# Kernel tuning notes

Hardware: AMD Instinct MI355X
Metric: run time of the kernel (lower is better)

The kernel has to match this reference:

```python
import jax, jax.numpy as jnp
import numpy as np

B, S, D, H, W = 2, 2048, 1024, 16, 256
HD = D // H

def setup_inputs() -> dict:
    key = jax.random.key(0)
    k1, k2, k3 = jax.random.split(key, 3)
    x = jax.random.normal(k1, (B, S, D), dtype=jnp.float32)
    w_qkv = jax.random.normal(k2, (D, 3 * D), dtype=jnp.float32) * (D ** -0.5)
    b_qkv = jnp.zeros((3 * D,), dtype=jnp.float32)
    w_out = jax.random.normal(k3, (D, D), dtype=jnp.float32) * (D ** -0.5)
    b_out = jnp.zeros((D,), dtype=jnp.float32)
    return {"x": x, "w_qkv": w_qkv, "b_qkv": b_qkv, "w_out": w_out, "b_out": b_out}

def reference(x, w_qkv, b_qkv, w_out, b_out):
    b, s, d = x.shape
    qkv = x @ w_qkv + b_qkv                       # [B,S,3D]
    qkv = qkv.reshape(b, s, 3, H, HD)
    q = jnp.transpose(qkv[:, :, 0], (0, 2, 1, 3))  # [B,H,S,HD]
    k = jnp.transpose(qkv[:, :, 1], (0, 2, 1, 3))
    v = jnp.transpose(qkv[:, :, 2], (0, 2, 1, 3))
    # NOTE: original scales by d_model**0.5, not head_dim**0.5
    scores = jnp.einsum('bhqd,bhkd->bhqk', q, k) / (d ** 0.5)
    idx = jnp.arange(s)
    band = jnp.abs(idx[:, None] - idx[None, :]) <= W  # |i-j| <= window_size
    scores = jnp.where(band[None, None], scores, -jnp.inf)
    attn = jax.nn.softmax(scores, axis=-1)
    out = jnp.einsum('bhqk,bhkd->bhqd', attn, v)
    out = jnp.transpose(out, (0, 2, 1, 3)).reshape(b, s, d)
    return out @ w_out + b_out
```

## Files before the change

### kernel.cpp

```cpp
#include <hip/hip_runtime.h>
#include <cstdint>
#include <cmath>

typedef unsigned short u16;
typedef __attribute__((ext_vector_type(8))) short bf16x8;
typedef __attribute__((ext_vector_type(4))) float f32x4;
typedef __attribute__((ext_vector_type(8))) unsigned short u16x8;

#define DEV static __device__ __forceinline__

DEV u16 f2bf(float f) {
  union { float f; uint32_t u; } v; v.f = f;
  uint32_t r = (v.u + 0x7fffu + ((v.u >> 16) & 1u)) >> 16;
  return (u16)r;
}

DEV float fexp2(float x) { return exp2f(x); }

DEV void async16(void* lds, const void* g) {
  __builtin_amdgcn_global_load_lds(
      (const __attribute__((address_space(1))) uint32_t*)g,
      (__attribute__((address_space(3))) uint32_t*)lds, 16, 0, 0);
}

__global__ void conv8(const float* __restrict__ in, u16* __restrict__ out, int n8) {
  int i = blockIdx.x * 256 + threadIdx.x;
  if (i >= n8) return;
  const float4* p = (const float4*)in + (size_t)i * 2;
  float4 a = p[0], b = p[1];
  u16x8 ov;
  ov[0] = f2bf(a.x); ov[1] = f2bf(a.y); ov[2] = f2bf(a.z); ov[3] = f2bf(a.w);
  ov[4] = f2bf(b.x); ov[5] = f2bf(b.y); ov[6] = f2bf(b.z); ov[7] = f2bf(b.w);
  *(u16x8*)(out + (size_t)i * 8) = ov;
}

__global__ void tconv(const float* __restrict__ in, u16* __restrict__ out, int R, int Cdim) {
  __shared__ float t[32][33];
  const int tx = threadIdx.x & 31, ty = threadIdx.x >> 5;
  const int r0 = blockIdx.y * 32, c0 = blockIdx.x * 32;
#pragma unroll
  for (int k = 0; k < 4; ++k) {
    int r = ty + k * 8;
    t[r][tx] = in[(size_t)(r0 + r) * Cdim + c0 + tx];
  }
  __syncthreads();
#pragma unroll
  for (int k = 0; k < 4; ++k) {
    int cc = ty + k * 8;
    out[(size_t)(c0 + cc) * R + r0 + tx] = f2bf(t[tx][cc]);
  }
}

template <int EPI>
__global__ __launch_bounds__(256, 2) void gemm_bt(
    const u16* __restrict__ A, const u16* __restrict__ BT,
    const float* __restrict__ bias, float* __restrict__ C,
    u16* __restrict__ qb, u16* __restrict__ kbuf, u16* __restrict__ vtb,
    int Mdim, int Ndim, int Kdim)
{
  __shared__ u16 Alds[128 * 64];
  __shared__ u16 Blds[128 * 64];
  const int tid = threadIdx.x;
  const int wid = tid >> 6, lane = tid & 63;
  const int g = lane >> 4, c = lane & 15;
  const int wr = wid >> 1, wc = wid & 1;
  const int gx = gridDim.x;
  const int nwg = gx * gridDim.y;
  const int lin = blockIdx.y * gx + blockIdx.x;
  const int work = (lin & 7) * (nwg >> 3) + (lin >> 3);
  const int row0 = (work / gx) * 128, col0 = (work % gx) * 128;

  f32x4 acc[4][4] = {};

  for (int kt = 0; kt < Kdim; kt += 64) {
    __syncthreads();
#pragma unroll
    for (int it = 0; it < 4; ++it) {
      int chunk = wid * 256 + it * 64 + lane;
      int r = chunk >> 3, j = chunk & 7;
      int js = j ^ (r & 7);
      async16((char*)Alds + (wid * 256 + it * 64) * 16,
              A + (size_t)(row0 + r) * Kdim + kt + js * 8);
      async16((char*)Blds + (wid * 256 + it * 64) * 16,
              BT + (size_t)(col0 + r) * Kdim + kt + js * 8);
    }
    __syncthreads();
#pragma unroll
    for (int kk = 0; kk < 2; ++kk) {
      bf16x8 av[4], bv[4];
#pragma unroll
      for (int mi = 0; mi < 4; ++mi) {
        int r = wr * 64 + mi * 16 + c;
        int js = (kk * 4 + g) ^ (r & 7);
        av[mi] = *(const bf16x8*)((const char*)Alds + r * 128 + js * 16);
      }
#pragma unroll
      for (int ni = 0; ni < 4; ++ni) {
        int r = wc * 64 + ni * 16 + c;
        int js = (kk * 4 + g) ^ (r & 7);
        bv[ni] = *(const bf16x8*)((const char*)Blds + r * 128 + js * 16);
      }
#pragma unroll
      for (int mi = 0; mi < 4; ++mi)
#pragma unroll
        for (int ni = 0; ni < 4; ++ni)
          acc[mi][ni] = __builtin_amdgcn_mfma_f32_16x16x32_bf16(
              av[mi], bv[ni], acc[mi][ni], 0, 0, 0);
    }
  }

#pragma unroll
  for (int mi = 0; mi < 4; ++mi) {
#pragma unroll
    for (int ni = 0; ni < 4; ++ni) {
      int colg = col0 + wc * 64 + ni * 16 + c;
      float bsv = bias[colg];
#pragma unroll
      for (int r = 0; r < 4; ++r) {
        int rowg = row0 + wr * 64 + mi * 16 + g * 4 + r;
        float val = acc[mi][ni][r] + bsv;
        if (EPI == 0) {
          C[(size_t)rowg * Ndim + colg] = val;
        } else {
          int t = colg >> 10, rem = colg & 1023;
          int h = rem >> 6, hd = rem & 63;
          int b = rowg >> 11, s = rowg & 2047;
          size_t bho = (size_t)(b * 16 + h);
          u16 bvv = f2bf(val);
          if (t == 0)      qb  [(bho * 2048 + s) * 64 + hd] = bvv;
          else if (t == 1) kbuf[(bho * 2048 + s) * 64 + hd] = bvv;
          else             vtb [(bho * 64 + hd) * 2048 + s] = bvv;
        }
      }
    }
  }
}

__global__ __launch_bounds__(512, 4) void attn_win(
    const u16* __restrict__ qb, const u16* __restrict__ kb,
    const u16* __restrict__ vtb, u16* __restrict__ hb)
{
  constexpr int S = 2048, W = 256;
  __shared__ u16 Klds[2][64 * 64];
  __shared__ u16 Vlds[2][64 * 64];
  __shared__ u16 Plds[8][16 * 64];

  const int tid = threadIdx.x, wid = tid >> 6, lane = tid & 63;
  const int g = lane >> 4, c = lane & 15;
  const int lin = blockIdx.x;
  const int work = (lin & 7) * 64 + (lin >> 3);
  const int qt = work & 15, bh = work >> 4;
  const int q0 = qt * 128;
  const int qr0 = q0 + wid * 16;
  const size_t bho = (size_t)bh * S * 64;

  bf16x8 aq[2];
  {
    const u16* qrow = qb + bho + (size_t)(qr0 + c) * 64;
    aq[0] = *(const bf16x8*)(qrow + g * 8);
    aq[1] = *(const bf16x8*)(qrow + 32 + g * 8);
  }
  f32x4 o[4] = {};
  float m[4] = {-1e30f, -1e30f, -1e30f, -1e30f};
  float lsum[4] = {0.f, 0.f, 0.f, 0.f};

  const int kstart = (q0 - W > 0) ? (q0 - W) : 0;
  const int kend = (q0 + 128 + W < S) ? (q0 + 128 + W) : S;
  constexpr float kS = 0.04508422002778011f;

  const int sr = tid >> 3, sj = tid & 7;
  const int sjs = sj ^ (sr & 7);
#define STAGE(buf, k0s)                                                         \
  {                                                                             \
    async16((char*)&Klds[buf][0] + tid * 16,                                    \
            kb + bho + (size_t)((k0s) + sr) * 64 + sjs * 8);                    \
    async16((char*)&Vlds[buf][0] + tid * 16,                                    \
            vtb + bho + (size_t)sr * S + (k0s) + sjs * 8);                      \
  }

  STAGE(0, kstart);
  asm volatile("s_waitcnt vmcnt(0)" ::: "memory");
  __syncthreads();

  int cur = 0;
  for (int k0 = kstart; k0 < kend; k0 += 64) {
    if (k0 + 64 < kend) STAGE(cur ^ 1, k0 + 64);

    const bool wave_active = !(k0 > qr0 + 15 + W) && !(k0 + 63 < qr0 - W);
    if (wave_active) {
      const u16* Kb = &Klds[cur][0];
      const u16* Vb = &Vlds[cur][0];

      f32x4 sacc[4] = {};
#pragma unroll
      for (int kb4 = 0; kb4 < 4; ++kb4) {
        int krow = kb4 * 16 + c;
#pragma unroll
        for (int kk = 0; kk < 2; ++kk) {
          int js = (kk * 4 + g) ^ (krow & 7);
          bf16x8 bk = *(const bf16x8*)((const char*)Kb + krow * 128 + js * 16);
          sacc[kb4] = __builtin_amdgcn_mfma_f32_16x16x32_bf16(aq[kk], bk, sacc[kb4], 0, 0, 0);
        }
      }

      const bool full = (k0 >= qr0 + 15 - W) && (k0 + 63 <= qr0 + W);
      float sl[4][4];
      if (full) {
#pragma unroll
        for (int kb4 = 0; kb4 < 4; ++kb4)
#pragma unroll
          for (int r = 0; r < 4; ++r) sl[kb4][r] = sacc[kb4][r] * kS;
      } else {
#pragma unroll
        for (int kb4 = 0; kb4 < 4; ++kb4) {
          int key = k0 + kb4 * 16 + c;
#pragma unroll
          for (int r = 0; r < 4; ++r) {
            int d = qr0 + g * 4 + r - key;
            bool valid = (d <= W) && (d >= -W);
            sl[kb4][r] = valid ? sacc[kb4][r] * kS : -1e30f;
          }
        }
      }

      float pmax[4];
#pragma unroll
      for (int r = 0; r < 4; ++r) {
        float mx = fmaxf(fmaxf(sl[0][r], sl[1][r]), fmaxf(sl[2][r], sl[3][r]));
        mx = fmaxf(mx, __shfl_xor(mx, 1));
        mx = fmaxf(mx, __shfl_xor(mx, 2));
        mx = fmaxf(mx, __shfl_xor(mx, 4));
        mx = fmaxf(mx, __shfl_xor(mx, 8));
        pmax[r] = mx;
      }
      float grow = fmaxf(fmaxf(pmax[0] - m[0], pmax[1] - m[1]),
                         fmaxf(pmax[2] - m[2], pmax[3] - m[3]));
      if (!__all(grow <= 8.0f)) {
#pragma unroll
        for (int r = 0; r < 4; ++r) {
          float mnew = fmaxf(m[r], pmax[r]);
          float fs = fexp2(m[r] - mnew);
          m[r] = mnew;
          lsum[r] *= fs;
          o[0][r] *= fs; o[1][r] *= fs; o[2][r] *= fs; o[3][r] *= fs;
        }
      }

      float rowsum[4] = {0.f, 0.f, 0.f, 0.f};
      u16* Pw = &Plds[wid][0];
#pragma unroll
      for (int kb4 = 0; kb4 < 4; ++kb4) {
#pragma unroll
        for (int r = 0; r < 4; ++r) {
          float p;
          if (full) {
            p = fexp2(sl[kb4][r] - m[r]);
          } else {
            p = (sl[kb4][r] > -1e29f) ? fexp2(sl[kb4][r] - m[r]) : 0.0f;
          }
          rowsum[r] += p;
          int row = g * 4 + r;
          int key = kb4 * 16 + c;
          int jsw = (key >> 3) ^ (row & 7);
          *((u16*)((char*)Pw + row * 128 + jsw * 16 + (key & 7) * 2)) = f2bf(p);
        }
      }
#pragma unroll
      for (int r = 0; r < 4; ++r) {
        float s2 = rowsum[r];
        s2 += __shfl_xor(s2, 1);
        s2 += __shfl_xor(s2, 2);
        s2 += __shfl_xor(s2, 4);
        s2 += __shfl_xor(s2, 8);
        lsum[r] += s2;
      }
      asm volatile("s_waitcnt lgkmcnt(0)" ::: "memory");
      __builtin_amdgcn_sched_barrier(0);
#pragma unroll
      for (int ks = 0; ks < 2; ++ks) {
        int js = (ks * 4 + g) ^ (c & 7);
        bf16x8 pa = *(const bf16x8*)((const char*)Pw + c * 128 + js * 16);
#pragma unroll
        for (int nb = 0; nb < 4; ++nb) {
          int hd = nb * 16 + c;
          int vjs = (ks * 4 + g) ^ (hd & 7);
          bf16x8 bv = *(const bf16x8*)((const char*)Vb + hd * 128 + vjs * 16);
          o[nb] = __builtin_amdgcn_mfma_f32_16x16x32_bf16(pa, bv, o[nb], 0, 0, 0);
        }
      }
    }

    asm volatile("s_waitcnt vmcnt(0)" ::: "memory");
    __syncthreads();
    cur ^= 1;
  }
#undef STAGE

  const int b = bh >> 4, h = bh & 15;
#pragma unroll
  for (int r = 0; r < 4; ++r) {
    float inv = 1.0f / lsum[r];
    int qr = qr0 + g * 4 + r;
#pragma unroll
    for (int nb = 0; nb < 4; ++nb) {
      int col = h * 64 + nb * 16 + c;
      hb[(size_t)(b * 2048 + qr) * 1024 + col] = f2bf(o[nb][r] * inv);
    }
  }
}

extern "C" void kernel_launch(void* const* d_in, const int* in_sizes, int n_in,
                              void* d_out, int out_size, void* d_ws, size_t ws_size,
                              hipStream_t stream) {
  const float* x     = (const float*)d_in[0];
  const float* w_qkv = (const float*)d_in[1];
  const float* b_qkv = (const float*)d_in[2];
  const float* w_out = (const float*)d_in[3];
  const float* b_out = (const float*)d_in[4];
  float* out = (float*)d_out;

  char* ws = (char*)d_ws;
  const size_t MB = 1024 * 1024;
  u16* xbf   = (u16*)(ws);
  u16* wqT   = (u16*)(ws + 8 * MB);
  u16* woT   = (u16*)(ws + 14 * MB);
  u16* qbuf  = (u16*)(ws + 16 * MB);
  u16* kbuf  = (u16*)(ws + 24 * MB);
  u16* vtbuf = (u16*)(ws + 32 * MB);
  u16* hbuf  = (u16*)(ws + 40 * MB);

  conv8<<<dim3(4096 * 1024 / 8 / 256), 256, 0, stream>>>(x, xbf, 4096 * 1024 / 8);
  tconv<<<dim3(3072 / 32, 1024 / 32), 256, 0, stream>>>(w_qkv, wqT, 1024, 3072);
  tconv<<<dim3(1024 / 32, 1024 / 32), 256, 0, stream>>>(w_out, woT, 1024, 1024);
  gemm_bt<1><<<dim3(3072 / 128, 4096 / 128), 256, 0, stream>>>(
      xbf, wqT, b_qkv, nullptr, qbuf, kbuf, vtbuf, 4096, 3072, 1024);
  attn_win<<<dim3(512), 512, 0, stream>>>(qbuf, kbuf, vtbuf, hbuf);
  gemm_bt<0><<<dim3(1024 / 128, 4096 / 128), 256, 0, stream>>>(
      hbuf, woT, b_out, out, nullptr, nullptr, nullptr, 4096, 1024, 1024);
}
```

Before: 182.7 us.

## Transpose QK^T MFMA so each lane owns one query row; fold scale into Q

Swaps the MFMA operands for the score product so each lane holds a single query row's scores. The row max then needs 2 cross-lane shuffles instead of 16, and the running max and sum become scalars per lane. The softmax scale is folded into Q in the QKV GEMM epilogue, and P is packed with v_cvt_pk_bf16_f32 into 8-byte LDS stores. It also raises wave priority around the MFMA blocks. In exchange, the rescale factors and final 1/l must be broadcast back to the output layout with __shfl, and Q picks up an extra bf16 rounding after scaling.

```diff
diff --git a/kernel.cpp b/kernel.cpp
--- a/kernel.cpp
+++ b/kernel.cpp
@@ -22,6 +22,8 @@
       (const __attribute__((address_space(1))) uint32_t*)g,
       (__attribute__((address_space(3))) uint32_t*)lds, 16, 0, 0);
 }
+
+#define QSCALE 0.04508422002778011f
 
 __global__ void conv8(const float* __restrict__ in, u16* __restrict__ out, int n8) {
   int i = blockIdx.x * 256 + threadIdx.x;
@@ -126,10 +128,9 @@
           int h = rem >> 6, hd = rem & 63;
           int b = rowg >> 11, s = rowg & 2047;
           size_t bho = (size_t)(b * 16 + h);
-          u16 bvv = f2bf(val);
-          if (t == 0)      qb  [(bho * 2048 + s) * 64 + hd] = bvv;
-          else if (t == 1) kbuf[(bho * 2048 + s) * 64 + hd] = bvv;
-          else             vtb [(bho * 64 + hd) * 2048 + s] = bvv;
+          if (t == 0)      qb  [(bho * 2048 + s) * 64 + hd] = f2bf(val * QSCALE);
+          else if (t == 1) kbuf[(bho * 2048 + s) * 64 + hd] = f2bf(val);
+          else             vtb [(bho * 64 + hd) * 2048 + s] = f2bf(val);
         }
       }
     }
@@ -152,21 +153,20 @@
   const int qt = work & 15, bh = work >> 4;
   const int q0 = qt * 128;
   const int qr0 = q0 + wid * 16;
+  const int qw = qr0 + c;
   const size_t bho = (size_t)bh * S * 64;
 
   bf16x8 aq[2];
   {
-    const u16* qrow = qb + bho + (size_t)(qr0 + c) * 64;
+    const u16* qrow = qb + bho + (size_t)qw * 64;
     aq[0] = *(const bf16x8*)(qrow + g * 8);
     aq[1] = *(const bf16x8*)(qrow + 32 + g * 8);
   }
   f32x4 o[4] = {};
-  float m[4] = {-1e30f, -1e30f, -1e30f, -1e30f};
-  float lsum[4] = {0.f, 0.f, 0.f, 0.f};
+  float m = -1e30f, lsum = 0.f;
 
   const int kstart = (q0 - W > 0) ? (q0 - W) : 0;
   const int kend = (q0 + 128 + W < S) ? (q0 + 128 + W) : S;
-  constexpr float kS = 0.04508422002778011f;
 
   const int sr = tid >> 3, sj = tid & 7;
   const int sjs = sj ^ (sr & 7);
@@ -192,6 +192,7 @@
       const u16* Vb = &Vlds[cur][0];
 
       f32x4 sacc[4] = {};
+      __builtin_amdgcn_s_setprio(1);
 #pragma unroll
       for (int kb4 = 0; kb4 < 4; ++kb4) {
         int krow = kb4 * 16 + c;
@@ -199,9 +200,10 @@
         for (int kk = 0; kk < 2; ++kk) {
           int js = (kk * 4 + g) ^ (krow & 7);
           bf16x8 bk = *(const bf16x8*)((const char*)Kb + krow * 128 + js * 16);
-          sacc[kb4] = __builtin_amdgcn_mfma_f32_16x16x32_bf16(aq[kk], bk, sacc[kb4], 0, 0, 0);
-        }
-      }
+          sacc[kb4] = __builtin_amdgcn_mfma_f32_16x16x32_bf16(bk, aq[kk], sacc[kb4], 0, 0, 0);
+        }
+      }
+      __builtin_amdgcn_s_setprio(0);
 
       const bool full = (k0 >= qr0 + 15 - W) && (k0 + 63 <= qr0 + W);
       float sl[4][4];
@@ -209,73 +211,72 @@
 #pragma unroll
         for (int kb4 = 0; kb4 < 4; ++kb4)
 #pragma unroll
-          for (int r = 0; r < 4; ++r) sl[kb4][r] = sacc[kb4][r] * kS;
+          for (int r = 0; r < 4; ++r) sl[kb4][r] = sacc[kb4][r];
       } else {
 #pragma unroll
         for (int kb4 = 0; kb4 < 4; ++kb4) {
-          int key = k0 + kb4 * 16 + c;
 #pragma unroll
           for (int r = 0; r < 4; ++r) {
-            int d = qr0 + g * 4 + r - key;
+            int key = k0 + kb4 * 16 + g * 4 + r;
+            int d = qw - key;
             bool valid = (d <= W) && (d >= -W);
-            sl[kb4][r] = valid ? sacc[kb4][r] * kS : -1e30f;
+            sl[kb4][r] = valid ? sacc[kb4][r] : -1e30f;
           }
         }
       }
 
-      float pmax[4];
-#pragma unroll
-      for (int r = 0; r < 4; ++r) {
-        float mx = fmaxf(fmaxf(sl[0][r], sl[1][r]), fmaxf(sl[2][r], sl[3][r]));
-        mx = fmaxf(mx, __shfl_xor(mx, 1));
-        mx = fmaxf(mx, __shfl_xor(mx, 2));
-        mx = fmaxf(mx, __shfl_xor(mx, 4));
-        mx = fmaxf(mx, __shfl_xor(mx, 8));
-        pmax[r] = mx;
-      }
-      float grow = fmaxf(fmaxf(pmax[0] - m[0], pmax[1] - m[1]),
-                         fmaxf(pmax[2] - m[2], pmax[3] - m[3]));
-      if (!__all(grow <= 8.0f)) {
-#pragma unroll
-        for (int r = 0; r < 4; ++r) {
-          float mnew = fmaxf(m[r], pmax[r]);
-          float fs = fexp2(m[r] - mnew);
-          m[r] = mnew;
-          lsum[r] *= fs;
-          o[0][r] *= fs; o[1][r] *= fs; o[2][r] *= fs; o[3][r] *= fs;
-        }
-      }
-
-      float rowsum[4] = {0.f, 0.f, 0.f, 0.f};
+      float mx = fmaxf(
+          fmaxf(fmaxf(fmaxf(sl[0][0], sl[0][1]), fmaxf(sl[0][2], sl[0][3])),
+                fmaxf(fmaxf(sl[1][0], sl[1][1]), fmaxf(sl[1][2], sl[1][3]))),
+          fmaxf(fmaxf(fmaxf(sl[2][0], sl[2][1]), fmaxf(sl[2][2], sl[2][3])),
+                fmaxf(fmaxf(sl[3][0], sl[3][1]), fmaxf(sl[3][2], sl[3][3]))));
+      mx = fmaxf(mx, __shfl_xor(mx, 16));
+      mx = fmaxf(mx, __shfl_xor(mx, 32));
+
+      if (!__all(mx - m <= 8.0f)) {
+        float mnew = fmaxf(m, mx);
+        float fs = fexp2(m - mnew);
+        m = mnew;
+        lsum *= fs;
+        float fsr[4];
+#pragma unroll
+        for (int r = 0; r < 4; ++r)
+          fsr[r] = __shfl(fs, (lane & 48) | (((lane & 48) >> 2) + r));
+#pragma unroll
+        for (int nb = 0; nb < 4; ++nb)
+#pragma unroll
+          for (int r = 0; r < 4; ++r) o[nb][r] *= fsr[r];
+      }
+
+      float rsum = 0.f;
       u16* Pw = &Plds[wid][0];
 #pragma unroll
       for (int kb4 = 0; kb4 < 4; ++kb4) {
-#pragma unroll
-        for (int r = 0; r < 4; ++r) {
-          float p;
-          if (full) {
-            p = fexp2(sl[kb4][r] - m[r]);
-          } else {
-            p = (sl[kb4][r] > -1e29f) ? fexp2(sl[kb4][r] - m[r]) : 0.0f;
-          }
-          rowsum[r] += p;
-          int row = g * 4 + r;
-          int key = kb4 * 16 + c;
-          int jsw = (key >> 3) ^ (row & 7);
-          *((u16*)((char*)Pw + row * 128 + jsw * 16 + (key & 7) * 2)) = f2bf(p);
-        }
-      }
-#pragma unroll
-      for (int r = 0; r < 4; ++r) {
-        float s2 = rowsum[r];
-        s2 += __shfl_xor(s2, 1);
-        s2 += __shfl_xor(s2, 2);
-        s2 += __shfl_xor(s2, 4);
-        s2 += __shfl_xor(s2, 8);
-        lsum[r] += s2;
-      }
+        float p0, p1, p2, p3;
+        if (full) {
+          p0 = fexp2(sl[kb4][0] - m); p1 = fexp2(sl[kb4][1] - m);
+          p2 = fexp2(sl[kb4][2] - m); p3 = fexp2(sl[kb4][3] - m);
+        } else {
+          p0 = (sl[kb4][0] > -1e29f) ? fexp2(sl[kb4][0] - m) : 0.f;
+          p1 = (sl[kb4][1] > -1e29f) ? fexp2(sl[kb4][1] - m) : 0.f;
+          p2 = (sl[kb4][2] > -1e29f) ? fexp2(sl[kb4][2] - m) : 0.f;
+          p3 = (sl[kb4][3] > -1e29f) ? fexp2(sl[kb4][3] - m) : 0.f;
+        }
+        rsum += (p0 + p1) + (p2 + p3);
+        uint32_t lo, hi;
+        asm("v_cvt_pk_bf16_f32 %0, %1, %2" : "=v"(lo) : "v"(p0), "v"(p1));
+        asm("v_cvt_pk_bf16_f32 %0, %1, %2" : "=v"(hi) : "v"(p2), "v"(p3));
+        uint2 wv; wv.x = lo; wv.y = hi;
+        *(uint2*)((char*)Pw + c * 128 + (((kb4 * 2 + (g >> 1)) ^ (c & 7)) << 4) +
+                  ((g & 1) << 3)) = wv;
+      }
+      rsum += __shfl_xor(rsum, 16);
+      rsum += __shfl_xor(rsum, 32);
+      lsum += rsum;
+
       asm volatile("s_waitcnt lgkmcnt(0)" ::: "memory");
       __builtin_amdgcn_sched_barrier(0);
+      __builtin_amdgcn_s_setprio(1);
 #pragma unroll
       for (int ks = 0; ks < 2; ++ks) {
         int js = (ks * 4 + g) ^ (c & 7);
@@ -288,6 +289,7 @@
           o[nb] = __builtin_amdgcn_mfma_f32_16x16x32_bf16(pa, bv, o[nb], 0, 0, 0);
         }
       }
+      __builtin_amdgcn_s_setprio(0);
     }
 
     asm volatile("s_waitcnt vmcnt(0)" ::: "memory");
@@ -297,14 +299,17 @@
 #undef STAGE
 
   const int b = bh >> 4, h = bh & 15;
+  float linv[4];
+#pragma unroll
+  for (int r = 0; r < 4; ++r)
+    linv[r] = 1.0f / __shfl(lsum, (lane & 48) | (((lane & 48) >> 2) + r));
 #pragma unroll
   for (int r = 0; r < 4; ++r) {
-    float inv = 1.0f / lsum[r];
     int qr = qr0 + g * 4 + r;
 #pragma unroll
     for (int nb = 0; nb < 4; ++nb) {
       int col = h * 64 + nb * 16 + c;
-      hb[(size_t)(b * 2048 + qr) * 1024 + col] = f2bf(o[nb][r] * inv);
+      hb[(size_t)(b * 2048 + qr) * 1024 + col] = f2bf(o[nb][r] * linv[r]);
     }
   }
 }
```

Result: faster. 169.5 us (-7.2%).
